# Performance work log

Hardware: AMD Instinct MI355X
Metric: run time of the kernel (lower is better)

Reference implementation:

```python
import jax, jax.numpy as jnp
import numpy as np
import math

L, B, D, H = 2048, 4, 1024, 16
DK = D // H
DFF = 4 * D
EPS = 1e-5


def setup_inputs() -> dict:
    key = jax.random.key(0)
    ks = jax.random.split(key, 16)
    s = 1.0 / math.sqrt(D)
    sf = 1.0 / math.sqrt(DFF)
    return {
        "x": jax.random.normal(ks[0], (L, B, D), jnp.float32),
        "Wq": jax.random.normal(ks[1], (D, D), jnp.float32) * s,
        "bq": jnp.zeros((D,), jnp.float32),
        "Wk": jax.random.normal(ks[2], (D, D), jnp.float32) * s,
        "bk": jnp.zeros((D,), jnp.float32),
        "Wv": jax.random.normal(ks[3], (D, D), jnp.float32) * s,
        "bv": jnp.zeros((D,), jnp.float32),
        "Wo": jax.random.normal(ks[4], (D, D), jnp.float32) * s,
        "bo": jnp.zeros((D,), jnp.float32),
        "W1": jax.random.normal(ks[5], (D, DFF), jnp.float32) * s,
        "b1": jnp.zeros((DFF,), jnp.float32),
        "W2": jax.random.normal(ks[6], (DFF, D), jnp.float32) * sf,
        "b2": jnp.zeros((D,), jnp.float32),
        "g1": jnp.ones((D,), jnp.float32),
        "be1": jnp.zeros((D,), jnp.float32),
        "g2": jnp.ones((D,), jnp.float32),
        "be2": jnp.zeros((D,), jnp.float32),
    }


def _layer_norm(x, g, b):
    mu = jnp.mean(x, axis=-1, keepdims=True)
    var = jnp.var(x, axis=-1, keepdims=True)
    return (x - mu) * jax.lax.rsqrt(var + EPS) * g + b


def reference(x, Wq, bq, Wk, bk, Wv, bv, Wo, bo, W1, b1, W2, b2, g1, be1, g2, be2):
    # x: (L, B, D)
    q = x @ Wq + bq
    k = x @ Wk + bk
    v = x @ Wv + bv
    # (L,B,H,dk) -> (B,H,L,dk)
    q = q.reshape(L, B, H, DK).transpose(1, 2, 0, 3)
    k = k.reshape(L, B, H, DK).transpose(1, 2, 0, 3)
    v = v.reshape(L, B, H, DK).transpose(1, 2, 0, 3)
    scale = 1.0 / math.sqrt(DK)
    scores = jnp.einsum('bhqd,bhkd->bhqk', q, k) * scale
    w = jax.nn.softmax(scores, axis=-1)
    attn = jnp.einsum('bhqk,bhkd->bhqd', w, v)  # (B,H,L,dk)
    attn = attn.transpose(2, 0, 1, 3).reshape(L, B, D)
    attn_out = attn @ Wo + bo
    x = _layer_norm(x + attn_out, g1, be1)
    h = jax.nn.gelu(x @ W1 + b1, approximate=False)
    ff = h @ W2 + b2
    return _layer_norm(x + ff, g2, be2)
```

## Files before the change

### kernel.cpp

```cpp
#include <hip/hip_runtime.h>

#define L_   2048
#define B_   4
#define D_   1024
#define H_   16
#define DK_  64
#define DFF_ 4096
#define NT_  (L_*B_)

typedef unsigned short u16;
typedef unsigned int   u32;
typedef __bf16 bf16x8 __attribute__((ext_vector_type(8)));
typedef float  f32x4  __attribute__((ext_vector_type(4)));

__device__ __forceinline__ u16 f2bf(float f) {
  u32 u = __float_as_uint(f);
  u += 0x7fffu + ((u >> 16) & 1u);
  return (u16)(u >> 16);
}
__device__ __forceinline__ float bf2f(u32 lo16) {
  return __uint_as_float(lo16 << 16);
}

#define GLDS16(g, l) __builtin_amdgcn_global_load_lds( \
    (const __attribute__((address_space(1))) void*)(g), \
    (__attribute__((address_space(3))) void*)(l), 16, 0, 0)

#define SCQ_ 0.18033688011112042f

__global__ __launch_bounds__(256) void transpose_w_k(
    const float* __restrict__ W, u16* __restrict__ Wt, int K, int N)
{
  __shared__ float tile[32][33];
  int n0 = blockIdx.x * 32, k0 = blockIdx.y * 32;
  int tx = threadIdx.x, ty = threadIdx.y;
#pragma unroll
  for (int i = ty; i < 32; i += 8)
    tile[i][tx] = W[(size_t)(k0 + i) * N + n0 + tx];
  __syncthreads();
#pragma unroll
  for (int i = ty; i < 32; i += 8)
    Wt[(size_t)(n0 + i) * K + k0 + tx] = f2bf(tile[tx][i]);
}

__global__ __launch_bounds__(256) void transpose_w4_k(
    const float* __restrict__ W0, const float* __restrict__ W1,
    const float* __restrict__ W2, const float* __restrict__ W3,
    u16* __restrict__ dst)
{
  __shared__ float tile[32][33];
  int z = blockIdx.z;
  const float* W = (z == 0) ? W0 : (z == 1) ? W1 : (z == 2) ? W2 : W3;
  u16* Wt = dst + (size_t)z * 1048576;
  int n0 = blockIdx.x * 32, k0 = blockIdx.y * 32;
  int tx = threadIdx.x, ty = threadIdx.y;
#pragma unroll
  for (int i = ty; i < 32; i += 8)
    tile[i][tx] = W[(size_t)(k0 + i) * 1024 + n0 + tx];
  __syncthreads();
#pragma unroll
  for (int i = ty; i < 32; i += 8)
    Wt[(size_t)(n0 + i) * 1024 + k0 + tx] = f2bf(tile[tx][i]);
}

__global__ __launch_bounds__(256) void f32_to_bf16_k(
    const float* __restrict__ in, u16* __restrict__ out, int n4)
{
  int i = blockIdx.x * 256 + threadIdx.x;
  if (i >= n4) return;
  float4 v = ((const float4*)in)[i];
  uint2 r;
  r.x = (u32)f2bf(v.x) | ((u32)f2bf(v.y) << 16);
  r.y = (u32)f2bf(v.z) | ((u32)f2bf(v.w) << 16);
  ((uint2*)out)[i] = r;
}

__global__ __launch_bounds__(256) void bias_concat_k(
    const float* __restrict__ bq, const float* __restrict__ bk,
    const float* __restrict__ bv, float* __restrict__ o)
{
  int i = blockIdx.x * 256 + threadIdx.x;
  float v = (i < 1024) ? bq[i] : ((i < 2048) ? bk[i - 1024] : bv[i - 2048]);
  o[i] = v;
}

template<int EPI>
__global__ __launch_bounds__(512, 2)
void gemm8(const u16* __restrict__ A, const u16* __restrict__ Bt,
           const float* __restrict__ bias, const void* __restrict__ res,
           u16* __restrict__ outb, int M, int N, int K)
{
  constexpr int BM = 256, BN = 256, BK = 64;
  constexpr int ABYTES = BM * BK * 2;
  constexpr int BUFB = (BM + BN) * BK * 2;
  constexpr int NGL = BUFB / 8192;
  __shared__ char SM[2 * BUFB];

  const int tid = threadIdx.x;
  const int w = tid >> 6, lane = tid & 63;
  const int l15 = lane & 15, l4 = lane >> 4;
  const int NK = K >> 6;

  const int gx = gridDim.x;
  int nwg = gx * gridDim.y;
  int id = blockIdx.y * gx + blockIdx.x;
  int q = nwg >> 3, r = nwg & 7;
  int xcd = id & 7, idx = id >> 3;
  int wg = (xcd < r ? xcd * (q + 1) : r * (q + 1) + (xcd - r) * q) + idx;
  const int m0 = (wg / gx) * BM, n0 = (wg % gx) * BN;
  const int wm = (w >> 2) * 128, wn = (w & 3) * 64;

  const u16* gsrc[NGL];
#pragma unroll
  for (int u = 0; u < NGL; ++u) {
    int o = u * 8192 + tid * 16;
    int row; const u16* base;
    if (o < ABYTES) { row = o >> 7; base = A + (size_t)(m0 + row) * K; }
    else { row = (o - ABYTES) >> 7; base = Bt + (size_t)(n0 + row) * K; }
    int col8 = ((o >> 4) & 7) ^ (row & 7);
    gsrc[u] = base + col8 * 8;
  }

  auto stage = [&](int tt, int u, char* dst) {
    GLDS16(gsrc[u] + (size_t)tt * BK, dst + u * 8192 + w * 1024);
  };

#pragma unroll
  for (int u = 0; u < NGL; ++u) stage(0, u, SM);
  asm volatile("s_waitcnt vmcnt(0)" ::: "memory");
  __builtin_amdgcn_s_barrier();

  f32x4 acc[8][4];
#pragma unroll
  for (int i = 0; i < 8; ++i)
#pragma unroll
    for (int j = 0; j < 4; ++j) acc[i][j] = (f32x4){0.f, 0.f, 0.f, 0.f};

  for (int t = 0; t < NK; ++t) {
    const char* rb = SM + (t & 1) * BUFB;
    char* wb = SM + ((t + 1) & 1) * BUFB;
    const int tt = (t + 1 < NK) ? t + 1 : 0;
    bf16x8 bfr[4];
#pragma unroll
    for (int ph = 0; ph < 4; ++ph) {
      const int kk = ph >> 1, mh = ph & 1;
      bf16x8 af[4];
#pragma unroll
      for (int mi = 0; mi < 4; ++mi) {
        int row = wm + mh * 64 + mi * 16 + l15;
        af[mi] = *(const bf16x8*)(rb + row * 128 +
                                  (((kk * 4 + l4) ^ (row & 7)) << 4));
      }
      if (mh == 0) {
#pragma unroll
        for (int nj = 0; nj < 4; ++nj) {
          int row = wn + nj * 16 + l15;
          bfr[nj] = *(const bf16x8*)(rb + ABYTES + row * 128 +
                                     (((kk * 4 + l4) ^ (row & 7)) << 4));
        }
      }
      if (ph == 0)      { stage(tt, 0, wb); stage(tt, 1, wb); stage(tt, 2, wb); }
      else if (ph == 1) { stage(tt, 3, wb); stage(tt, 4, wb); stage(tt, 5, wb); }
      else if (ph == 2) { stage(tt, 6, wb); stage(tt, 7, wb); }
      __builtin_amdgcn_s_barrier();
      asm volatile("s_waitcnt lgkmcnt(0)" ::: "memory");
      __builtin_amdgcn_sched_barrier(0);
      __builtin_amdgcn_s_setprio(1);
#pragma unroll
      for (int mi = 0; mi < 4; ++mi)
#pragma unroll
        for (int nj = 0; nj < 4; ++nj)
          acc[mh * 4 + mi][nj] = __builtin_amdgcn_mfma_f32_16x16x32_bf16(
              af[mi], bfr[nj], acc[mh * 4 + mi][nj], 0, 0, 0);
      __builtin_amdgcn_s_setprio(0);
      if (ph == 3)
        asm volatile("s_waitcnt vmcnt(0)" ::: "memory");
      __builtin_amdgcn_s_barrier();
    }
  }
  asm volatile("s_waitcnt vmcnt(0)" ::: "memory");

  const int gm = m0 + wm + l4 * 4;
  const int gn = n0 + wn + l15;
#pragma unroll
  for (int mi = 0; mi < 8; ++mi) {
#pragma unroll
    for (int nj = 0; nj < 4; ++nj) {
      int col = gn + nj * 16;
      float bv = bias[col];
#pragma unroll
      for (int rr = 0; rr < 4; ++rr) {
        int row = gm + mi * 16 + rr;
        float v = acc[mi][nj][rr] + bv;
        if (EPI == 2) {
          float gv = 0.5f * v * (1.f + erff(v * 0.70710678118654752f));
          outb[(size_t)row * N + col] = f2bf(gv);
        } else if (EPI == 3) {
          int which = col >> 10, c1 = col & 1023;
          int ll = row >> 2, bb = row & 3;
          int hh = c1 >> 6, dd = c1 & 63;
          if (which == 0) v *= SCQ_;
          outb[(size_t)which * 8388608 +
               ((((size_t)(bb * H_ + hh)) * L_ + ll) << 6) + dd] = f2bf(v);
        } else if (EPI == 5) {
          size_t idxo = (size_t)row * N + col;
          outb[idxo] = f2bf(v + ((const float*)res)[idxo]);
        } else {
          size_t idxo = (size_t)row * N + col;
          outb[idxo] = f2bf(v + bf2f(((const u16*)res)[idxo]));
        }
      }
    }
  }
}

template<int EPI>
__global__ __launch_bounds__(512, 2)
void gemm_pipe(const u16* __restrict__ A, const u16* __restrict__ Bt,
               const float* __restrict__ bias, const void* __restrict__ res,
               u16* __restrict__ outb, int M, int N, int K)
{
  constexpr int BM = 256, BN = 128, BK = 64;
  constexpr int ABYTES = BM * BK * 2;
  constexpr int BUFB = (BM + BN) * BK * 2;
  __shared__ char SM[3 * BUFB];

  const int tid = threadIdx.x;
  const int w = tid >> 6, lane = tid & 63;
  const int l15 = lane & 15, l4 = lane >> 4;
  const int NK = K >> 6;

  const int gx = gridDim.x;
  int nwg = gx * gridDim.y;
  int id = blockIdx.y * gx + blockIdx.x;
  int q = nwg >> 3, r = nwg & 7;
  int xcd = id & 7, idx = id >> 3;
  int wg = (xcd < r ? xcd * (q + 1) : r * (q + 1) + (xcd - r) * q) + idx;
  const int m0 = (wg / gx) * BM, n0 = (wg % gx) * BN;
  const int wm = (w >> 1) * 64, wn = (w & 1) * 64;

  const u16* gsrc[6];
#pragma unroll
  for (int u = 0; u < 6; ++u) {
    int o = u * 8192 + tid * 16;
    int row; const u16* base;
    if (o < ABYTES) {
      row = o >> 7;
      base = A + (size_t)(m0 + row) * K;
    } else {
      int ob = o - ABYTES;
      row = ob >> 7;
      base = Bt + (size_t)(n0 + row) * K;
    }
    int col8 = ((o >> 4) & 7) ^ (row & 7);
    gsrc[u] = base + col8 * 8;
  }

  auto stage = [&](int t, int u) {
    const u16* s = gsrc[u] + (size_t)((t < NK) ? t : 0) * BK;
    GLDS16(s, SM + (t % 3) * BUFB + u * 8192 + w * 1024);
  };

  for (int tt = 0; tt < 2; ++tt)
#pragma unroll
    for (int u = 0; u < 6; ++u) stage(tt, u);
  asm volatile("s_waitcnt vmcnt(6)" ::: "memory");
  asm volatile("s_barrier" ::: "memory");

  f32x4 acc[4][4];
#pragma unroll
  for (int i = 0; i < 4; ++i)
#pragma unroll
    for (int j = 0; j < 4; ++j) acc[i][j] = (f32x4){0.f, 0.f, 0.f, 0.f};

  for (int t = 0; t < NK; ++t) {
    const char* rb = SM + (t % 3) * BUFB;
    const int tn = t + 2;
#pragma unroll
    for (int ph = 0; ph < 2; ++ph) {
      bf16x8 af[4], bfr[4];
#pragma unroll
      for (int mi = 0; mi < 4; ++mi) {
        int row = wm + mi * 16 + l15;
        af[mi] = *(const bf16x8*)(rb + row * 128 +
                                  (((ph * 4 + l4) ^ (l15 & 7)) << 4));
      }
      stage(tn, ph * 3 + 0);
#pragma unroll
      for (int nj = 0; nj < 4; ++nj) {
        int row = wn + nj * 16 + l15;
        bfr[nj] = *(const bf16x8*)(rb + ABYTES + row * 128 +
                                   (((ph * 4 + l4) ^ (l15 & 7)) << 4));
      }
      stage(tn, ph * 3 + 1);
      stage(tn, ph * 3 + 2);
      __builtin_amdgcn_s_setprio(1);
#pragma unroll
      for (int mi = 0; mi < 4; ++mi)
#pragma unroll
        for (int nj = 0; nj < 4; ++nj)
          acc[mi][nj] = __builtin_amdgcn_mfma_f32_16x16x32_bf16(
              af[mi], bfr[nj], acc[mi][nj], 0, 0, 0);
      __builtin_amdgcn_s_setprio(0);
    }
    asm volatile("s_waitcnt lgkmcnt(0)" ::: "memory");
    asm volatile("s_waitcnt vmcnt(6)" ::: "memory");
    asm volatile("s_barrier" ::: "memory");
  }
  asm volatile("s_waitcnt vmcnt(0)" ::: "memory");

  const int gm = m0 + wm + l4 * 4;
  const int gn = n0 + wn + l15;
#pragma unroll
  for (int mi = 0; mi < 4; ++mi) {
#pragma unroll
    for (int nj = 0; nj < 4; ++nj) {
      int col = gn + nj * 16;
      float bv = bias[col];
#pragma unroll
      for (int rr = 0; rr < 4; ++rr) {
        int row = gm + mi * 16 + rr;
        float v = acc[mi][nj][rr] + bv;
        if (EPI == 5) {
          size_t idxo = (size_t)row * N + col;
          outb[idxo] = f2bf(v + ((const float*)res)[idxo]);
        } else {
          size_t idxo = (size_t)row * N + col;
          outb[idxo] = f2bf(v + bf2f(((const u16*)res)[idxo]));
        }
      }
    }
  }
}

__global__ __launch_bounds__(256, 3)
void attn_fwd2(const u16* __restrict__ qp, const u16* __restrict__ kp,
               const u16* __restrict__ vp, u16* __restrict__ op)
{
  __shared__ u16 Ks[2][64 * 64];
  __shared__ u16 Vt[2][64 * 64];
  const int tid = threadIdx.x, w = tid >> 6, lane = tid & 63;
  const int l15 = lane & 15, l4 = lane >> 4;
  const int n = blockIdx.x;
  const int bh = (n & 7) | ((n >> 7) << 3);
  const int qi = (n >> 3) & 15;
  const int q0 = qi * 128;
  const u16* qb = qp + (size_t)bh * L_ * DK_;
  const u16* kb = kp + (size_t)bh * L_ * DK_;
  const u16* vb = vp + (size_t)bh * L_ * DK_;

  bf16x8 qf[2][2];
#pragma unroll
  for (int g = 0; g < 2; ++g)
#pragma unroll
    for (int kk = 0; kk < 2; ++kk)
      qf[g][kk] = *(const bf16x8*)&qb[(size_t)(q0 + g * 64 + w * 16 + l15) * DK_ +
                                      kk * 32 + l4 * 8];

  f32x4 accO[2][4];
  f32x4 lacc[2];
#pragma unroll
  for (int g = 0; g < 2; ++g) {
#pragma unroll
    for (int i = 0; i < 4; ++i) accO[g][i] = (f32x4){0.f, 0.f, 0.f, 0.f};
    lacc[g] = (f32x4){0.f, 0.f, 0.f, 0.f};
  }

  bf16x8 oneb;
  {
    u32 ob = (l15 == 0) ? 0x3f803f80u : 0u;
#pragma unroll
    for (int j = 0; j < 4; ++j) ((u32*)&oneb)[j] = ob;
  }

  int rho0 = tid >> 3, rho1 = (256 + tid) >> 3, cseg = lane & 7;
  int kv0 = (rho0 & 32) | ((rho0 & 12) << 1) | ((rho0 & 16) >> 2) | (rho0 & 3);
  int kv1 = (rho1 & 32) | ((rho1 & 12) << 1) | ((rho1 & 16) >> 2) | (rho1 & 3);
  const u16* ksrc0 = kb + (size_t)kv0 * DK_ + ((cseg ^ (rho0 & 7)) << 3);
  const u16* ksrc1 = kb + (size_t)kv1 * DK_ + ((cseg ^ (rho1 & 7)) << 3);

  const int vseg = tid & 7, vkvp = tid >> 3;
  const u16* vsrc = vb + (size_t)(vkvp * 2) * DK_ + vseg * 8;
  u32 voff[8];
#pragma unroll
  for (int dd2 = 0; dd2 < 4; ++dd2) {
    int d0 = vseg * 8 + dd2 * 2, d1 = d0 + 1;
    voff[dd2 * 2] = d0 * 128 +
        ((((vkvp >> 2) ^ (d0 & 7) ^ (d0 >> 3)) << 4) | ((vkvp & 3) << 2));
    voff[dd2 * 2 + 1] = d1 * 128 +
        ((((vkvp >> 2) ^ (d1 & 7) ^ (d1 >> 3)) << 4) | ((vkvp & 3) << 2));
  }

  auto packV = [&](int buf, uint4 a, uint4 b) {
#pragma unroll
    for (int dd2 = 0; dd2 < 4; ++dd2) {
      u32 ai = ((const u32*)&a)[dd2], bi = ((const u32*)&b)[dd2];
      *(u32*)((char*)Vt[buf] + voff[dd2 * 2])     = __builtin_amdgcn_perm(bi, ai, 0x05040100u);
      *(u32*)((char*)Vt[buf] + voff[dd2 * 2 + 1]) = __builtin_amdgcn_perm(bi, ai, 0x07060302u);
    }
  };

  auto exp_pack = [&](f32x4 (&s)[4], u32 (&pk)[2][4]) {
#pragma unroll
    for (int i = 0; i < 4; ++i)
#pragma unroll
      for (int rr = 0; rr < 4; ++rr) s[i][rr] = exp2f(s[i][rr]);
#pragma unroll
    for (int kk = 0; kk < 2; ++kk)
#pragma unroll
      for (int j2 = 0; j2 < 4; ++j2) {
        int nb = kk * 2 + (j2 >> 1);
        int rr = (j2 & 1) * 2;
        u32 rres;
        asm("v_cvt_pk_bf16_f32 %0, %1, %2" : "=v"(rres)
            : "v"(s[nb][rr]), "v"(s[nb][rr + 1]));
        pk[kk][j2] = rres;
      }
  };

  {
    uint4 a = *(const uint4*)vsrc;
    uint4 b = *(const uint4*)(vsrc + DK_);
    GLDS16(ksrc0, &Ks[0][w * 512]);
    GLDS16(ksrc1, &Ks[0][2048 + w * 512]);
    packV(0, a, b);
  }
  __syncthreads();

  constexpr int NTI = L_ / 64;
  for (int t = 0; t < NTI; ++t) {
    const int cur = t & 1;
    const bool pf = (t + 1 < NTI);
    const int tn = pf ? t + 1 : t;

    uint4 va = *(const uint4*)(vsrc + (size_t)(tn * 64) * DK_);
    uint4 vbv = *(const uint4*)(vsrc + (size_t)(tn * 64) * DK_ + DK_);
    if (pf) {
      GLDS16(ksrc0 + (size_t)((t + 1) * 64) * DK_, &Ks[cur ^ 1][w * 512]);
      GLDS16(ksrc1 + (size_t)((t + 1) * 64) * DK_, &Ks[cur ^ 1][2048 + w * 512]);
    }

    f32x4 s0[4], s1[4];
#pragma unroll
    for (int i = 0; i < 4; ++i) {
      s0[i] = (f32x4){0.f, 0.f, 0.f, 0.f};
      s1[i] = (f32x4){0.f, 0.f, 0.f, 0.f};
    }
#pragma unroll
    for (int kk = 0; kk < 2; ++kk) {
#pragma unroll
      for (int nb = 0; nb < 4; ++nb) {
        int row = nb * 16 + l15;
        bf16x8 kf = *(const bf16x8*)((const char*)Ks[cur] + row * 128 +
                                     (((kk * 4 + l4) ^ (row & 7)) << 4));
        s0[nb] = __builtin_amdgcn_mfma_f32_16x16x32_bf16(kf, qf[0][kk], s0[nb], 0, 0, 0);
        s1[nb] = __builtin_amdgcn_mfma_f32_16x16x32_bf16(kf, qf[1][kk], s1[nb], 0, 0, 0);
      }
    }

    u32 pk0[2][4], pk1[2][4];
    exp_pack(s0, pk0);
    exp_pack(s1, pk1);

    if (pf) packV(cur ^ 1, va, vbv);

#pragma unroll
    for (int kk = 0; kk < 2; ++kk) {
      bf16x8 pa0, pa1;
      ((u32*)&pa0)[0] = pk0[kk][0]; ((u32*)&pa0)[1] = pk0[kk][1];
      ((u32*)&pa0)[2] = pk0[kk][2]; ((u32*)&pa0)[3] = pk0[kk][3];
      ((u32*)&pa1)[0] = pk1[kk][0]; ((u32*)&pa1)[1] = pk1[kk][1];
      ((u32*)&pa1)[2] = pk1[kk][2]; ((u32*)&pa1)[3] = pk1[kk][3];
      lacc[0] = __builtin_amdgcn_mfma_f32_16x16x32_bf16(pa0, oneb, lacc[0], 0, 0, 0);
      lacc[1] = __builtin_amdgcn_mfma_f32_16x16x32_bf16(pa1, oneb, lacc[1], 0, 0, 0);
#pragma unroll
      for (int nb2 = 0; nb2 < 4; ++nb2) {
        int drow = nb2 * 16 + l15;
        bf16x8 vf = *(const bf16x8*)((const char*)Vt[cur] + drow * 128 +
                                     (((kk * 4 + l4) ^ (drow & 7) ^ (drow >> 3)) << 4));
        accO[0][nb2] = __builtin_amdgcn_mfma_f32_16x16x32_bf16(pa0, vf, accO[0][nb2], 0, 0, 0);
        accO[1][nb2] = __builtin_amdgcn_mfma_f32_16x16x32_bf16(pa1, vf, accO[1][nb2], 0, 0, 0);
      }
    }
    __syncthreads();
  }

  const int bb = bh >> 4, hh = bh & 15;
#pragma unroll
  for (int g = 0; g < 2; ++g) {
#pragma unroll
    for (int rr = 0; rr < 4; ++rr) {
      float ls = __shfl(lacc[g][rr], l4 << 4);
      float rl = 1.f / ls;
      int qg = q0 + g * 64 + w * 16 + l4 * 4 + rr;
      size_t base = ((size_t)qg * B_ + bb) * D_ + hh * 64;
#pragma unroll
      for (int nb2 = 0; nb2 < 4; ++nb2)
        op[base + nb2 * 16 + l15] = f2bf(accO[g][nb2][rr] * rl);
    }
  }
}

__global__ __launch_bounds__(256) void layernorm_bf_k(
    const u16* __restrict__ y, const float* __restrict__ g, const float* __restrict__ be,
    float* __restrict__ of, u16* __restrict__ ob)
{
  int row = blockIdx.x, tid = threadIdx.x;
  uint2 raw = *(const uint2*)&y[(size_t)row * D_ + tid * 4];
  float v0 = bf2f(raw.x & 0xffffu), v1 = bf2f(raw.x >> 16);
  float v2 = bf2f(raw.y & 0xffffu), v3 = bf2f(raw.y >> 16);
  float s = (v0 + v1) + (v2 + v3);
  float ss = v0 * v0 + v1 * v1 + v2 * v2 + v3 * v3;
#pragma unroll
  for (int msk = 32; msk >= 1; msk >>= 1) {
    s += __shfl_xor(s, msk);
    ss += __shfl_xor(ss, msk);
  }
  __shared__ float rs[4], rss[4];
  if ((tid & 63) == 0) { rs[tid >> 6] = s; rss[tid >> 6] = ss; }
  __syncthreads();
  s = rs[0] + rs[1] + rs[2] + rs[3];
  ss = rss[0] + rss[1] + rss[2] + rss[3];
  float mu = s * (1.f / D_);
  float var = ss * (1.f / D_) - mu * mu;
  float rstd = rsqrtf(var + 1e-5f);
  int c = tid * 4;
  float o0 = (v0 - mu) * rstd * g[c + 0] + be[c + 0];
  float o1 = (v1 - mu) * rstd * g[c + 1] + be[c + 1];
  float o2 = (v2 - mu) * rstd * g[c + 2] + be[c + 2];
  float o3 = (v3 - mu) * rstd * g[c + 3] + be[c + 3];
  if (of) {
    float4 o = {o0, o1, o2, o3};
    *(float4*)&of[(size_t)row * D_ + c] = o;
  }
  if (ob) {
    uint2 r;
    r.x = (u32)f2bf(o0) | ((u32)f2bf(o1) << 16);
    r.y = (u32)f2bf(o2) | ((u32)f2bf(o3) << 16);
    *(uint2*)&ob[(size_t)row * D_ + c] = r;
  }
}

extern "C" void kernel_launch(void* const* d_in, const int* in_sizes, int n_in,
                              void* d_out, int out_size, void* d_ws, size_t ws_size,
                              hipStream_t stream)
{
  const float* x   = (const float*)d_in[0];
  const float* Wq  = (const float*)d_in[1];
  const float* bq  = (const float*)d_in[2];
  const float* Wk  = (const float*)d_in[3];
  const float* bk  = (const float*)d_in[4];
  const float* Wv  = (const float*)d_in[5];
  const float* bv  = (const float*)d_in[6];
  const float* Wo  = (const float*)d_in[7];
  const float* bo  = (const float*)d_in[8];
  const float* W1f = (const float*)d_in[9];
  const float* b1  = (const float*)d_in[10];
  const float* W2f = (const float*)d_in[11];
  const float* b2  = (const float*)d_in[12];
  const float* g1  = (const float*)d_in[13];
  const float* be1 = (const float*)d_in[14];
  const float* g2  = (const float*)d_in[15];
  const float* be2 = (const float*)d_in[16];

  char* ws = (char*)d_ws;
  const size_t MB = 1024 * 1024;
  u16* WqT  = (u16*)(ws + 0 * MB);
  u16* WoT  = (u16*)(ws + 6 * MB);
  u16* W1T  = (u16*)(ws + 8 * MB);
  u16* W2T  = (u16*)(ws + 16 * MB);
  u16* xb   = (u16*)(ws + 24 * MB);
  u16* qp   = (u16*)(ws + 40 * MB);
  u16* astd = (u16*)(ws + 88 * MB);
  u16* yb   = (u16*)(ws + 104 * MB);
  u16* x1b  = (u16*)(ws + 120 * MB);
  u16* hbuf = (u16*)(ws + 136 * MB);
  float* bcat = (float*)(ws + 200 * MB);
  u16* kp = qp + 8388608;
  u16* vp = qp + 16777216;

  dim3 tb(32, 8);
  transpose_w4_k<<<dim3(32, 32, 4), tb, 0, stream>>>(Wq, Wk, Wv, Wo, WqT);
  transpose_w_k<<<dim3(128, 32), tb, 0, stream>>>(W1f, W1T, D_, DFF_);
  transpose_w_k<<<dim3(32, 128), tb, 0, stream>>>(W2f, W2T, DFF_, D_);
  f32_to_bf16_k<<<NT_ * D_ / 4 / 256, 256, 0, stream>>>(x, xb, NT_ * D_ / 4);
  bias_concat_k<<<12, 256, 0, stream>>>(bq, bk, bv, bcat);

  gemm8<3><<<dim3(12, 32), 512, 0, stream>>>(
      xb, WqT, bcat, nullptr, qp, NT_, 3072, D_);

  attn_fwd2<<<1024, 256, 0, stream>>>(qp, kp, vp, astd);

  gemm_pipe<5><<<dim3(8, 32), 512, 0, stream>>>(
      astd, WoT, bo, x, yb, NT_, D_, D_);
  layernorm_bf_k<<<NT_, 256, 0, stream>>>(yb, g1, be1, nullptr, x1b);
  gemm8<2><<<dim3(16, 32), 512, 0, stream>>>(
      x1b, W1T, b1, nullptr, hbuf, NT_, DFF_, D_);
  gemm_pipe<6><<<dim3(8, 32), 512, 0, stream>>>(
      hbuf, W2T, b2, x1b, yb, NT_, D_, DFF_);
  layernorm_bf_k<<<NT_, 256, 0, stream>>>(yb, g2, be2, (float*)d_out, nullptr);
}
```

Before: 439.7 us.

## Double attention block size to 512 threads covering 256 queries per block

The attention kernel now runs 512-thread blocks that each handle 256 query rows, so every K/V tile loaded into shared memory serves twice as many queries. Each thread loads half as much K and V per tile, which cuts global and LDS staging traffic per query. The softmax exponent also switches from exp2f to the raw hardware exp2 builtin. In exchange the grid drops to 512 blocks, which lowers the number of resident waves available to hide latency.

```diff
diff --git a/kernel.cpp b/kernel.cpp
--- a/kernel.cpp
+++ b/kernel.cpp
@@ -333,7 +333,7 @@
   }
 }
 
-__global__ __launch_bounds__(256, 3)
+__global__ __launch_bounds__(512, 2)
 void attn_fwd2(const u16* __restrict__ qp, const u16* __restrict__ kp,
                const u16* __restrict__ vp, u16* __restrict__ op)
 {
@@ -342,9 +342,9 @@
   const int tid = threadIdx.x, w = tid >> 6, lane = tid & 63;
   const int l15 = lane & 15, l4 = lane >> 4;
   const int n = blockIdx.x;
-  const int bh = (n & 7) | ((n >> 7) << 3);
-  const int qi = (n >> 3) & 15;
-  const int q0 = qi * 128;
+  const int bh = (n & 7) | ((n >> 6) << 3);
+  const int qi = (n >> 3) & 7;
+  const int q0 = qi * 256;
   const u16* qb = qp + (size_t)bh * L_ * DK_;
   const u16* kb = kp + (size_t)bh * L_ * DK_;
   const u16* vb = vp + (size_t)bh * L_ * DK_;
@@ -354,7 +354,7 @@
   for (int g = 0; g < 2; ++g)
 #pragma unroll
     for (int kk = 0; kk < 2; ++kk)
-      qf[g][kk] = *(const bf16x8*)&qb[(size_t)(q0 + g * 64 + w * 16 + l15) * DK_ +
+      qf[g][kk] = *(const bf16x8*)&qb[(size_t)(q0 + g * 128 + w * 16 + l15) * DK_ +
                                       kk * 32 + l4 * 8];
 
   f32x4 accO[2][4];
@@ -373,38 +373,32 @@
     for (int j = 0; j < 4; ++j) ((u32*)&oneb)[j] = ob;
   }
 
-  int rho0 = tid >> 3, rho1 = (256 + tid) >> 3, cseg = lane & 7;
+  int rho0 = tid >> 3, cseg = tid & 7;
   int kv0 = (rho0 & 32) | ((rho0 & 12) << 1) | ((rho0 & 16) >> 2) | (rho0 & 3);
-  int kv1 = (rho1 & 32) | ((rho1 & 12) << 1) | ((rho1 & 16) >> 2) | (rho1 & 3);
   const u16* ksrc0 = kb + (size_t)kv0 * DK_ + ((cseg ^ (rho0 & 7)) << 3);
-  const u16* ksrc1 = kb + (size_t)kv1 * DK_ + ((cseg ^ (rho1 & 7)) << 3);
-
-  const int vseg = tid & 7, vkvp = tid >> 3;
-  const u16* vsrc = vb + (size_t)(vkvp * 2) * DK_ + vseg * 8;
-  u32 voff[8];
-#pragma unroll
-  for (int dd2 = 0; dd2 < 4; ++dd2) {
-    int d0 = vseg * 8 + dd2 * 2, d1 = d0 + 1;
-    voff[dd2 * 2] = d0 * 128 +
-        ((((vkvp >> 2) ^ (d0 & 7) ^ (d0 >> 3)) << 4) | ((vkvp & 3) << 2));
-    voff[dd2 * 2 + 1] = d1 * 128 +
-        ((((vkvp >> 2) ^ (d1 & 7) ^ (d1 >> 3)) << 4) | ((vkvp & 3) << 2));
-  }
-
-  auto packV = [&](int buf, uint4 a, uint4 b) {
-#pragma unroll
-    for (int dd2 = 0; dd2 < 4; ++dd2) {
-      u32 ai = ((const u32*)&a)[dd2], bi = ((const u32*)&b)[dd2];
-      *(u32*)((char*)Vt[buf] + voff[dd2 * 2])     = __builtin_amdgcn_perm(bi, ai, 0x05040100u);
-      *(u32*)((char*)Vt[buf] + voff[dd2 * 2 + 1]) = __builtin_amdgcn_perm(bi, ai, 0x07060302u);
-    }
+
+  const int vdg = tid & 15, vkvp = tid >> 4;
+  const u16* vsrc = vb + (size_t)(vkvp * 2) * DK_ + vdg * 4;
+  u32 voff[4];
+#pragma unroll
+  for (int dd = 0; dd < 4; ++dd) {
+    int d = vdg * 4 + dd;
+    voff[dd] = d * 128 +
+        ((((vkvp >> 2) ^ (d & 7) ^ (d >> 3)) << 4) | ((vkvp & 3) << 2));
+  }
+
+  auto packV = [&](int buf, uint2 a, uint2 b) {
+    *(u32*)((char*)Vt[buf] + voff[0]) = __builtin_amdgcn_perm(b.x, a.x, 0x05040100u);
+    *(u32*)((char*)Vt[buf] + voff[1]) = __builtin_amdgcn_perm(b.x, a.x, 0x07060302u);
+    *(u32*)((char*)Vt[buf] + voff[2]) = __builtin_amdgcn_perm(b.y, a.y, 0x05040100u);
+    *(u32*)((char*)Vt[buf] + voff[3]) = __builtin_amdgcn_perm(b.y, a.y, 0x07060302u);
   };
 
   auto exp_pack = [&](f32x4 (&s)[4], u32 (&pk)[2][4]) {
 #pragma unroll
     for (int i = 0; i < 4; ++i)
 #pragma unroll
-      for (int rr = 0; rr < 4; ++rr) s[i][rr] = exp2f(s[i][rr]);
+      for (int rr = 0; rr < 4; ++rr) s[i][rr] = __builtin_amdgcn_exp2f(s[i][rr]);
 #pragma unroll
     for (int kk = 0; kk < 2; ++kk)
 #pragma unroll
@@ -419,10 +413,9 @@
   };
 
   {
-    uint4 a = *(const uint4*)vsrc;
-    uint4 b = *(const uint4*)(vsrc + DK_);
+    uint2 a = *(const uint2*)vsrc;
+    uint2 b = *(const uint2*)(vsrc + DK_);
     GLDS16(ksrc0, &Ks[0][w * 512]);
-    GLDS16(ksrc1, &Ks[0][2048 + w * 512]);
     packV(0, a, b);
   }
   __syncthreads();
@@ -433,12 +426,10 @@
     const bool pf = (t + 1 < NTI);
     const int tn = pf ? t + 1 : t;
 
-    uint4 va = *(const uint4*)(vsrc + (size_t)(tn * 64) * DK_);
-    uint4 vbv = *(const uint4*)(vsrc + (size_t)(tn * 64) * DK_ + DK_);
-    if (pf) {
+    uint2 va = *(const uint2*)(vsrc + (size_t)(tn * 64) * DK_);
+    uint2 vbv = *(const uint2*)(vsrc + (size_t)(tn * 64) * DK_ + DK_);
+    if (pf)
       GLDS16(ksrc0 + (size_t)((t + 1) * 64) * DK_, &Ks[cur ^ 1][w * 512]);
-      GLDS16(ksrc1 + (size_t)((t + 1) * 64) * DK_, &Ks[cur ^ 1][2048 + w * 512]);
-    }
 
     f32x4 s0[4], s1[4];
 #pragma unroll
@@ -492,7 +483,7 @@
     for (int rr = 0; rr < 4; ++rr) {
       float ls = __shfl(lacc[g][rr], l4 << 4);
       float rl = 1.f / ls;
-      int qg = q0 + g * 64 + w * 16 + l4 * 4 + rr;
+      int qg = q0 + g * 128 + w * 16 + l4 * 4 + rr;
       size_t base = ((size_t)qg * B_ + bb) * D_ + hh * 64;
 #pragma unroll
       for (int nb2 = 0; nb2 < 4; ++nb2)
@@ -589,7 +580,7 @@
   gemm8<3><<<dim3(12, 32), 512, 0, stream>>>(
       xb, WqT, bcat, nullptr, qp, NT_, 3072, D_);
 
-  attn_fwd2<<<1024, 256, 0, stream>>>(qp, kp, vp, astd);
+  attn_fwd2<<<512, 512, 0, stream>>>(qp, kp, vp, astd);
 
   gemm_pipe<5><<<dim3(8, 32), 512, 0, stream>>>(
       astd, WoT, bo, x, yb, NT_, D_, D_);
```

New measurement: 421.6 us. 4.1% less time.
